# Optimization experiments

Hardware: AMD Instinct MI355X
Metric: run time of the kernel (lower is better)

Reference implementation:

```python
import jax, jax.numpy as jnp
import numpy as np

B, N, M = 8, 512, 6          # batch, num_roads, max_action
ED, SRC, OBS = 8, 64, 32     # edge_dim, source_obs_dim, obs_dim
D, H = 16, 64                # out_dim (fixed in source), MLPBase hidden


def setup_inputs() -> dict:
    key = jax.random.key(0)
    ks = jax.random.split(key, 24)
    p = lambda k, sh, s=0.05: (jax.random.normal(k, sh) * s).astype(jnp.float32)
    inp = {}
    inp['obs'] = jax.random.normal(ks[0], (B, SRC), dtype=jnp.float32)
    inp['obs_all'] = jax.random.normal(ks[1], (B, N, OBS), dtype=jnp.float32)
    inp['edge_attrs'] = jax.random.normal(ks[2], (B, N, N, ED), dtype=jnp.float32)
    inp['ridxs'] = jax.random.randint(ks[3], (B,), 0, N)
    idxs = jax.random.randint(ks[4], (N, M), 0, N)
    masks = jax.random.randint(ks[5], (N, M), 0, 2)
    inp['road_neighbor_idxs'] = idxs
    inp['road_neighbor_masks'] = masks
    # A[i, j] = 1 iff i is a (masked-valid) neighbor of j
    cols = jnp.repeat(jnp.arange(N), M)
    inp['A'] = jnp.zeros((N, N), jnp.float32).at[idxs.reshape(-1), cols].max(
        masks.reshape(-1).astype(jnp.float32))
    inp['PA'] = jnp.full((N, N), 1e-6, jnp.float32)
    # parameters (stored as (in, out); y = x @ W + b)
    inp['w_src'] = p(ks[6], (SRC, D * M)); inp['b_src'] = jnp.zeros((D * M,), jnp.float32)
    inp['w_obs'] = p(ks[7], (OBS, D));     inp['b_obs'] = jnp.zeros((D,), jnp.float32)
    inp['res_w'] = p(ks[8], (2, D, D));    inp['res_b'] = jnp.zeros((2, D), jnp.float32)
    inp['ge_we'] = p(ks[9], (2, ED, D));   inp['ge_be'] = jnp.zeros((2, D), jnp.float32)
    inp['ge_wemb'] = p(ks[10], (2, 3 * D, D)); inp['ge_bemb'] = jnp.zeros((2, D), jnp.float32)
    inp['gated_w'] = p(ks[11], (2 * D * M, 2 * D)); inp['gated_b'] = jnp.zeros((2 * D,), jnp.float32)
    inp['base_w1'] = p(ks[12], (D, H));    inp['base_b1'] = jnp.zeros((H,), jnp.float32)
    inp['base_w2'] = p(ks[13], (H, H));    inp['base_b2'] = jnp.zeros((H,), jnp.float32)
    inp['act_w'] = p(ks[14], (H, M));      inp['act_b'] = jnp.zeros((M,), jnp.float32)
    return inp


def _edge_conv_gat(x, edge_attrs, adj, we, be, wemb, bemb):
    """EdgeConvGat: emb(cat[x_i, x_j, edge_map(e)]) aggregated by adj.
    emb is linear, so split its weight and avoid the (B,N,N,3D) concat:
      sum_j adj[bij] * (x_i W1 + x_j W2 + e_ij W3 + b)
    """
    W1, W2, W3 = wemb[:D], wemb[D:2 * D], wemb[2 * D:]
    e = edge_attrs @ we + be                      # (B,N,N,D)
    ep = e @ W3                                   # (B,N,N,D)
    deg = adj.sum(-1)                             # (B,N) row-sums of adj
    return ((x @ W1) * deg[..., None]
            + jnp.einsum('bij,bjk->bik', adj, x @ W2)
            + jnp.einsum('bij,bijk->bik', adj, ep)
            + bemb * deg[..., None])


def reference(obs, obs_all, edge_attrs, ridxs, road_neighbor_idxs,
              road_neighbor_masks, A, PA, w_src, b_src, w_obs, b_obs,
              res_w, res_b, ge_we, ge_be, ge_wemb, ge_bemb,
              gated_w, gated_b, base_w1, base_b1, base_w2, base_b2,
              act_w, act_b):
    # source_obs_map / obs_map (mean_field=1 -> full obs_all)
    obs_p = obs @ w_src + b_src                   # (B, D*M)
    x = obs_all @ w_obs + b_obs                   # (B, N, D)
    # adaptive adjacency (training=False -> dropout is identity)
    adj = jnp.broadcast_to(A + PA, (obs.shape[0], N, N))
    # graph conv loop (source overwrites obs_all_adaptive each iter from the
    # same x, faithfully reproduced; only the last iteration feeds the output)
    x_adapt = x
    for i in range(2):
        res = x @ res_w[i] + res_b[i]
        agg = _edge_conv_gat(x, edge_attrs, adj, ge_we[i], ge_be[i],
                             ge_wemb[i], ge_bemb[i])
        x_adapt = jax.nn.relu(res + agg)
    # gather per-road neighbor features and mask invalid slots to -1
    idx = road_neighbor_idxs[ridxs]               # (B, M)
    mask = road_neighbor_masks[ridxs]             # (B, M)
    sel = jnp.take_along_axis(x_adapt, idx[:, :, None], axis=1)  # (B, M, D)
    sel = jnp.where(mask[..., None] == 0, -1.0, sel).reshape(obs.shape[0], -1)
    # gated fusion + MLPBase (2-layer MLP stand-in) + action head
    g = jnp.concatenate([obs_p, sel], axis=-1) @ gated_w + gated_b
    gated, gate = jnp.split(g, 2, axis=-1)
    h = gated * jax.nn.sigmoid(gate)
    h = jax.nn.relu(h @ base_w1 + base_b1)
    h = jax.nn.relu(h @ base_w2 + base_b2)        # F.relu(self.base(...))
    return h @ act_w + act_b                      # (B, M) action values
```

## Files before the change

### kernel.cpp

```cpp
#include <hip/hip_runtime.h>
#include <math.h>


constexpr int Bc   = 8;
constexpr int Nc   = 512;
constexpr int Mc   = 6;
constexpr int EDc  = 8;
constexpr int SRCc = 64;
constexpr int OBSc = 32;
constexpr int Dc   = 16;
constexpr int Hc   = 64;

__global__ __launch_bounds__(512) void anmodel_kernel(
    const float* __restrict__ obs,
    const float* __restrict__ obs_all,
    const float* __restrict__ edge_attrs,
    const int*   __restrict__ ridxs,
    const int*   __restrict__ rni,
    const int*   __restrict__ rnm,
    const float* __restrict__ A,
    const float* __restrict__ PA,
    const float* __restrict__ w_src,
    const float* __restrict__ b_src,
    const float* __restrict__ w_obs,
    const float* __restrict__ b_obs,
    const float* __restrict__ res_w,
    const float* __restrict__ res_b,
    const float* __restrict__ ge_we,
    const float* __restrict__ ge_be,
    const float* __restrict__ ge_wemb,
    const float* __restrict__ ge_bemb,
    const float* __restrict__ gated_w,
    const float* __restrict__ gated_b,
    const float* __restrict__ base_w1,
    const float* __restrict__ base_b1,
    const float* __restrict__ base_w2,
    const float* __restrict__ base_b2,
    const float* __restrict__ act_w,
    const float* __restrict__ act_b,
    float* __restrict__ out)
{
    const int b    = blockIdx.x;
    const int tid  = threadIdx.x;
    const int lane = tid & 63;
    const int wave = tid >> 6;

    __shared__ float s_x[Nc][Dc];
    __shared__ float s_w[Mc][Nc];
    __shared__ float s_wobs[OBSc][Dc];
    __shared__ float s_bobs[Dc];
    __shared__ float s_W1[Dc][Dc];
    __shared__ float s_W2[Dc][Dc];
    __shared__ float s_resw[Dc][Dc];
    __shared__ float s_resb[Dc];
    __shared__ float s_we3[EDc][Dc];
    __shared__ float s_be3[Dc];
    __shared__ float s_bemb[Dc];
    __shared__ int   s_idx[Mc];
    __shared__ int   s_msk[Mc];
    __shared__ float s_sel[Mc * Dc];
    __shared__ float s_obsp[SRCc + 32];
    __shared__ float s_h0[Dc];
    __shared__ float s_h1[Hc];
    __shared__ float s_h2[Hc];

    const float* wemb1 = ge_wemb + 3 * Dc * Dc;
    for (int t = tid; t < OBSc * Dc; t += 512) s_wobs[t / Dc][t % Dc] = w_obs[t];
    for (int t = tid; t < Dc; t += 512) {
        s_bobs[t] = b_obs[t];
        s_resb[t] = res_b[Dc + t];
        s_bemb[t] = ge_bemb[Dc + t];
        float acc = 0.f;
        #pragma unroll
        for (int k = 0; k < Dc; ++k)
            acc = fmaf(ge_be[Dc + k], wemb1[(2 * Dc + k) * Dc + t], acc);
        s_be3[t] = acc;
    }
    for (int t = tid; t < Dc * Dc; t += 512) {
        s_W1[t / Dc][t % Dc]   = wemb1[t];
        s_W2[t / Dc][t % Dc]   = wemb1[Dc * Dc + t];
        s_resw[t / Dc][t % Dc] = res_w[Dc * Dc + t];
    }
    for (int t = tid; t < EDc * Dc; t += 512) {
        const int e = t / Dc, d = t % Dc;
        float acc = 0.f;
        #pragma unroll
        for (int k = 0; k < Dc; ++k)
            acc = fmaf(ge_we[EDc * Dc + e * Dc + k], wemb1[(2 * Dc + k) * Dc + d], acc);
        s_we3[e][d] = acc;
    }
    if (tid < Mc) {
        const int r = ridxs[b];
        s_idx[tid] = rni[r * Mc + tid];
        s_msk[tid] = rnm[r * Mc + tid];
    }
    __syncthreads();

    {
        const int j = tid;
        const float* oa = obs_all + ((size_t)b * Nc + j) * OBSc;
        float o[OBSc];
        #pragma unroll
        for (int k = 0; k < OBSc; k += 4) {
            const float4 v = *reinterpret_cast<const float4*>(oa + k);
            o[k] = v.x; o[k + 1] = v.y; o[k + 2] = v.z; o[k + 3] = v.w;
        }
        float xv[Dc];
        #pragma unroll
        for (int d = 0; d < Dc; ++d) xv[d] = s_bobs[d];
        #pragma unroll
        for (int k = 0; k < OBSc; ++k) {
            const float ok = o[k];
            #pragma unroll
            for (int d = 0; d < Dc; ++d) xv[d] = fmaf(ok, s_wobs[k][d], xv[d]);
        }
        #pragma unroll
        for (int d = 0; d < Dc; ++d) s_x[j][d] = xv[d];
    }
    #pragma unroll
    for (int m = 0; m < Mc; ++m) {
        const int i = s_idx[m];
        s_w[m][tid] = A[(size_t)i * Nc + tid] + PA[(size_t)i * Nc + tid];
    }
    __syncthreads();

    if (wave < Mc) {
        const int m = wave;
        const float* __restrict__ wrow = &s_w[m][0];

        float dv = 0.f;
        #pragma unroll
        for (int t = 0; t < Nc / 64; ++t) dv += wrow[t * 64 + lane];
        #pragma unroll
        for (int s = 1; s < 64; s <<= 1) dv += __shfl_xor(dv, s);

        const int dq = lane & 15, jg = lane >> 4;
        float wx = 0.f;
        #pragma unroll 8
        for (int t = 0; t < Nc / 4; ++t) {
            const int j = t * 4 + jg;
            wx = fmaf(wrow[j], s_x[j][dq], wx);
        }
        wx += __shfl_xor(wx, 16);
        wx += __shfl_xor(wx, 32);
        float wxv[Dc];
        #pragma unroll
        for (int k = 0; k < Dc; ++k) wxv[k] = __shfl(wx, k);

        const int e8 = lane & 7, jg8 = lane >> 3;
        const int i  = s_idx[m];
        const float* __restrict__ Erow = edge_attrs + (((size_t)b * Nc + i) * Nc) * EDc;
        float ag = 0.f;
        #pragma unroll 4
        for (int t = 0; t < Nc / 8; ++t) {
            const int j = t * 8 + jg8;
            ag = fmaf(wrow[j], Erow[(size_t)j * EDc + e8], ag);
        }
        ag += __shfl_xor(ag, 8);
        ag += __shfl_xor(ag, 16);
        ag += __shfl_xor(ag, 32);
        float agv[EDc];
        #pragma unroll
        for (int e = 0; e < EDc; ++e) agv[e] = __shfl(ag, e);

        if (lane < Dc) {
            const int d = lane;
            float resv = s_resb[d];
            float w1t  = 0.f;
            float adot = 0.f;
            #pragma unroll
            for (int k = 0; k < Dc; ++k) {
                const float xik = s_x[i][k];
                resv = fmaf(xik, s_resw[k][d], resv);
                w1t  = fmaf(xik, s_W1[k][d], w1t);
                adot = fmaf(wxv[k], s_W2[k][d], adot);
            }
            float agdot = 0.f;
            #pragma unroll
            for (int e = 0; e < EDc; ++e) agdot = fmaf(agv[e], s_we3[e][d], agdot);
            float aggv = fmaf(w1t, dv, adot) + agdot + dv * (s_be3[d] + s_bemb[d]);
            float xa = resv + aggv;
            xa = xa > 0.f ? xa : 0.f;
            s_sel[m * Dc + d] = (s_msk[m] == 0) ? -1.0f : xa;
        }
    } else {
        const int t = (wave - 6) * 64 + lane;
        if (t < SRCc + 32) {
            float acc = b_src[t];
            #pragma unroll 8
            for (int s = 0; s < SRCc; ++s)
                acc = fmaf(obs[b * SRCc + s], w_src[s * 96 + t], acc);
            s_obsp[t] = acc;
        }
    }
    __syncthreads();

    if (wave == 0) {
        float gv = 0.f;
        if (lane < 32) {
            gv = gated_b[lane];
            for (int t = 0; t < 96; ++t) gv = fmaf(s_obsp[t], gated_w[t * 32 + lane], gv);
            for (int t = 0; t < 96; ++t) gv = fmaf(s_sel[t],  gated_w[(96 + t) * 32 + lane], gv);
        }
        const float gate = __shfl(gv, (lane & 15) + 16);
        if (lane < Dc) {
            s_h0[lane] = gv * (1.0f / (1.0f + expf(-gate)));
        }
    }
    __syncthreads();
    if (wave == 0) {
        float acc = base_b1[lane];
        #pragma unroll
        for (int k = 0; k < Dc; ++k) acc = fmaf(s_h0[k], base_w1[k * Hc + lane], acc);
        s_h1[lane] = acc > 0.f ? acc : 0.f;
    }
    __syncthreads();
    if (wave == 0) {
        float acc = base_b2[lane];
        #pragma unroll
        for (int k = 0; k < Hc; ++k) acc = fmaf(s_h1[k], base_w2[k * Hc + lane], acc);
        s_h2[lane] = acc > 0.f ? acc : 0.f;
    }
    __syncthreads();
    if (wave == 0 && lane < Mc) {
        float acc = act_b[lane];
        #pragma unroll
        for (int k = 0; k < Hc; ++k) acc = fmaf(s_h2[k], act_w[k * Mc + lane], acc);
        out[b * Mc + lane] = acc;
    }
}

extern "C" void kernel_launch(void* const* d_in, const int* in_sizes, int n_in,
                              void* d_out, int out_size, void* d_ws, size_t ws_size,
                              hipStream_t stream) {
    (void)in_sizes; (void)n_in; (void)d_ws; (void)ws_size; (void)out_size;
    anmodel_kernel<<<dim3(Bc), dim3(512), 0, stream>>>(
        (const float*)d_in[0],  (const float*)d_in[1],  (const float*)d_in[2],
        (const int*)  d_in[3],  (const int*)  d_in[4],  (const int*)  d_in[5],
        (const float*)d_in[6],  (const float*)d_in[7],  (const float*)d_in[8],
        (const float*)d_in[9],  (const float*)d_in[10], (const float*)d_in[11],
        (const float*)d_in[12], (const float*)d_in[13], (const float*)d_in[14],
        (const float*)d_in[15], (const float*)d_in[16], (const float*)d_in[17],
        (const float*)d_in[18], (const float*)d_in[19], (const float*)d_in[20],
        (const float*)d_in[21], (const float*)d_in[22], (const float*)d_in[23],
        (const float*)d_in[24], (const float*)d_in[25],
        (float*)d_out);
}
```

Measured before the change: 151.9 us.

## Split into per-(batch,slot) row kernel and small head kernel, reassociate obs projection

Replaces the single 8-block kernel with a 48-block kernel, one block per (batch, neighbor slot), that computes each selected row's graph-conv output. A second 8-block kernel then runs the gated fusion and MLP head. The row kernel also reorders the algebra: it aggregates raw obs_all weighted by the adjacency row and projects that sum through w_obs once, instead of projecting all 512 nodes first. This spreads the work over more CUs and cuts FMA work. The cost is a second launch and a workspace round-trip, and each block now re-reads obs_all for its batch.

```diff
diff --git a/kernel.cpp b/kernel.cpp
--- a/kernel.cpp
+++ b/kernel.cpp
@@ -11,8 +11,7 @@
 constexpr int Dc   = 16;
 constexpr int Hc   = 64;
 
-__global__ __launch_bounds__(512) void anmodel_kernel(
-    const float* __restrict__ obs,
+__global__ __launch_bounds__(256) void an_rows_kernel(
     const float* __restrict__ obs_all,
     const float* __restrict__ edge_attrs,
     const int*   __restrict__ ridxs,
@@ -20,8 +19,6 @@
     const int*   __restrict__ rnm,
     const float* __restrict__ A,
     const float* __restrict__ PA,
-    const float* __restrict__ w_src,
-    const float* __restrict__ b_src,
     const float* __restrict__ w_obs,
     const float* __restrict__ b_obs,
     const float* __restrict__ res_w,
@@ -30,6 +27,130 @@
     const float* __restrict__ ge_be,
     const float* __restrict__ ge_wemb,
     const float* __restrict__ ge_bemb,
+    float* __restrict__ sel_out)
+{
+    const int blk = blockIdx.x;
+    const int b   = blk / Mc;
+    const int m   = blk % Mc;
+    const int tid = threadIdx.x;
+
+    __shared__ float s_w[Nc];
+    __shared__ float s_woa[8][OBSc];
+    __shared__ float s_ag[32][EDc];
+    __shared__ float s_oai[OBSc];
+    __shared__ float s_woaf[OBSc];
+    __shared__ float s_agf[EDc];
+    __shared__ float s_xi[Dc];
+    __shared__ float s_wx[Dc];
+    __shared__ float s_q[Dc];
+    __shared__ float s_deg;
+    __shared__ int   s_i, s_mk;
+
+    if (tid == 0) {
+        const int r = ridxs[b];
+        s_i  = rni[r * Mc + m];
+        s_mk = rnm[r * Mc + m];
+    }
+    __syncthreads();
+    const int i = s_i;
+
+    for (int t = tid; t < Nc; t += 256)
+        s_w[t] = A[(size_t)i * Nc + t] + PA[(size_t)i * Nc + t];
+    if (tid < OBSc)
+        s_oai[tid] = obs_all[((size_t)b * Nc + i) * OBSc + tid];
+    __syncthreads();
+
+    {
+        const int d = tid & 31, jg = tid >> 5;
+        const float* __restrict__ oab = obs_all + (size_t)b * Nc * OBSc;
+        float acc = 0.f;
+        #pragma unroll 4
+        for (int t = 0; t < Nc / 8; ++t) {
+            const int j = t * 8 + jg;
+            acc = fmaf(s_w[j], oab[(size_t)j * OBSc + d], acc);
+        }
+        s_woa[jg][d] = acc;
+    }
+    {
+        const int e = tid & 7, jg = tid >> 3;
+        const float* __restrict__ Erow = edge_attrs + ((size_t)b * Nc + i) * Nc * EDc;
+        float acc = 0.f;
+        #pragma unroll 4
+        for (int t = 0; t < Nc / 32; ++t) {
+            const int j = t * 32 + jg;
+            acc = fmaf(s_w[j], Erow[(size_t)j * EDc + e], acc);
+        }
+        s_ag[jg][e] = acc;
+    }
+    if (tid < 64) {
+        float dv = 0.f;
+        #pragma unroll
+        for (int t = 0; t < Nc / 64; ++t) dv += s_w[t * 64 + tid];
+        #pragma unroll
+        for (int s = 1; s < 64; s <<= 1) dv += __shfl_xor(dv, s);
+        if (tid == 0) s_deg = dv;
+    }
+    __syncthreads();
+
+    const float deg = s_deg;
+    if (tid < OBSc) {
+        float acc = 0.f;
+        #pragma unroll
+        for (int g = 0; g < 8; ++g) acc += s_woa[g][tid];
+        s_woaf[tid] = acc;
+    } else if (tid >= 64 && tid < 64 + EDc) {
+        const int e = tid - 64;
+        float acc = 0.f;
+        #pragma unroll
+        for (int g = 0; g < 32; ++g) acc += s_ag[g][e];
+        s_agf[e] = acc;
+    } else if (tid >= 128 && tid < 128 + Dc) {
+        const int d = tid - 128;
+        float acc = b_obs[d];
+        #pragma unroll 8
+        for (int k = 0; k < OBSc; ++k) acc = fmaf(s_oai[k], w_obs[k * Dc + d], acc);
+        s_xi[d] = acc;
+    }
+    __syncthreads();
+
+    if (tid < Dc) {
+        const int d = tid;
+        float acc = deg * b_obs[d];
+        #pragma unroll 8
+        for (int k = 0; k < OBSc; ++k) acc = fmaf(s_woaf[k], w_obs[k * Dc + d], acc);
+        s_wx[d] = acc;
+    } else if (tid >= 64 && tid < 64 + Dc) {
+        const int d = tid - 64;
+        float acc = deg * ge_be[Dc + d];
+        #pragma unroll
+        for (int e = 0; e < EDc; ++e)
+            acc = fmaf(s_agf[e], ge_we[EDc * Dc + e * Dc + d], acc);
+        s_q[d] = acc;
+    }
+    __syncthreads();
+
+    if (tid < Dc) {
+        const int d = tid;
+        const float* __restrict__ wemb1 = ge_wemb + 3 * Dc * Dc;
+        float resv = res_b[Dc + d];
+        float acc  = deg * ge_bemb[Dc + d];
+        #pragma unroll
+        for (int k = 0; k < Dc; ++k) {
+            resv = fmaf(s_xi[k], res_w[Dc * Dc + k * Dc + d], resv);
+            acc  = fmaf(deg * s_xi[k], wemb1[k * Dc + d], acc);
+            acc  = fmaf(s_wx[k],       wemb1[(Dc + k) * Dc + d], acc);
+            acc  = fmaf(s_q[k],        wemb1[(2 * Dc + k) * Dc + d], acc);
+        }
+        float xa = resv + acc;
+        xa = xa > 0.f ? xa : 0.f;
+        sel_out[((size_t)b * Mc + m) * Dc + d] = (s_mk == 0) ? -1.0f : xa;
+    }
+}
+
+__global__ __launch_bounds__(128) void an_head_kernel(
+    const float* __restrict__ obs,
+    const float* __restrict__ w_src,
+    const float* __restrict__ b_src,
     const float* __restrict__ gated_w,
     const float* __restrict__ gated_b,
     const float* __restrict__ base_w1,
@@ -38,211 +159,75 @@
     const float* __restrict__ base_b2,
     const float* __restrict__ act_w,
     const float* __restrict__ act_b,
+    const float* __restrict__ sel_in,
     float* __restrict__ out)
 {
-    const int b    = blockIdx.x;
-    const int tid  = threadIdx.x;
-    const int lane = tid & 63;
-    const int wave = tid >> 6;
-
-    __shared__ float s_x[Nc][Dc];
-    __shared__ float s_w[Mc][Nc];
-    __shared__ float s_wobs[OBSc][Dc];
-    __shared__ float s_bobs[Dc];
-    __shared__ float s_W1[Dc][Dc];
-    __shared__ float s_W2[Dc][Dc];
-    __shared__ float s_resw[Dc][Dc];
-    __shared__ float s_resb[Dc];
-    __shared__ float s_we3[EDc][Dc];
-    __shared__ float s_be3[Dc];
-    __shared__ float s_bemb[Dc];
-    __shared__ int   s_idx[Mc];
-    __shared__ int   s_msk[Mc];
-    __shared__ float s_sel[Mc * Dc];
-    __shared__ float s_obsp[SRCc + 32];
-    __shared__ float s_h0[Dc];
-    __shared__ float s_h1[Hc];
-    __shared__ float s_h2[Hc];
-
-    const float* wemb1 = ge_wemb + 3 * Dc * Dc;
-    for (int t = tid; t < OBSc * Dc; t += 512) s_wobs[t / Dc][t % Dc] = w_obs[t];
-    for (int t = tid; t < Dc; t += 512) {
-        s_bobs[t] = b_obs[t];
-        s_resb[t] = res_b[Dc + t];
-        s_bemb[t] = ge_bemb[Dc + t];
-        float acc = 0.f;
-        #pragma unroll
-        for (int k = 0; k < Dc; ++k)
-            acc = fmaf(ge_be[Dc + k], wemb1[(2 * Dc + k) * Dc + t], acc);
-        s_be3[t] = acc;
-    }
-    for (int t = tid; t < Dc * Dc; t += 512) {
-        s_W1[t / Dc][t % Dc]   = wemb1[t];
-        s_W2[t / Dc][t % Dc]   = wemb1[Dc * Dc + t];
-        s_resw[t / Dc][t % Dc] = res_w[Dc * Dc + t];
-    }
-    for (int t = tid; t < EDc * Dc; t += 512) {
-        const int e = t / Dc, d = t % Dc;
-        float acc = 0.f;
-        #pragma unroll
-        for (int k = 0; k < Dc; ++k)
-            acc = fmaf(ge_we[EDc * Dc + e * Dc + k], wemb1[(2 * Dc + k) * Dc + d], acc);
-        s_we3[e][d] = acc;
-    }
+    const int b   = blockIdx.x;
+    const int tid = threadIdx.x;
+    __shared__ float s_sel[96], s_obsp[96], s_g[32], s_h0[Dc], s_h1[Hc], s_h2[Hc];
+
+    if (tid < 96) {
+        s_sel[tid] = sel_in[b * 96 + tid];
+        float acc = b_src[tid];
+        #pragma unroll 8
+        for (int s = 0; s < SRCc; ++s)
+            acc = fmaf(obs[b * SRCc + s], w_src[s * 96 + tid], acc);
+        s_obsp[tid] = acc;
+    }
+    __syncthreads();
+    if (tid < 32) {
+        float gv = gated_b[tid];
+        for (int t = 0; t < 96; ++t) gv = fmaf(s_obsp[t], gated_w[t * 32 + tid], gv);
+        for (int t = 0; t < 96; ++t) gv = fmaf(s_sel[t],  gated_w[(96 + t) * 32 + tid], gv);
+        s_g[tid] = gv;
+    }
+    __syncthreads();
+    if (tid < Dc)
+        s_h0[tid] = s_g[tid] * (1.0f / (1.0f + expf(-s_g[tid + Dc])));
+    __syncthreads();
+    if (tid < Hc) {
+        float acc = base_b1[tid];
+        #pragma unroll
+        for (int k = 0; k < Dc; ++k) acc = fmaf(s_h0[k], base_w1[k * Hc + tid], acc);
+        s_h1[tid] = acc > 0.f ? acc : 0.f;
+    }
+    __syncthreads();
+    if (tid < Hc) {
+        float acc = base_b2[tid];
+        #pragma unroll 8
+        for (int k = 0; k < Hc; ++k) acc = fmaf(s_h1[k], base_w2[k * Hc + tid], acc);
+        s_h2[tid] = acc > 0.f ? acc : 0.f;
+    }
+    __syncthreads();
     if (tid < Mc) {
-        const int r = ridxs[b];
-        s_idx[tid] = rni[r * Mc + tid];
-        s_msk[tid] = rnm[r * Mc + tid];
-    }
-    __syncthreads();
-
-    {
-        const int j = tid;
-        const float* oa = obs_all + ((size_t)b * Nc + j) * OBSc;
-        float o[OBSc];
-        #pragma unroll
-        for (int k = 0; k < OBSc; k += 4) {
-            const float4 v = *reinterpret_cast<const float4*>(oa + k);
-            o[k] = v.x; o[k + 1] = v.y; o[k + 2] = v.z; o[k + 3] = v.w;
-        }
-        float xv[Dc];
-        #pragma unroll
-        for (int d = 0; d < Dc; ++d) xv[d] = s_bobs[d];
-        #pragma unroll
-        for (int k = 0; k < OBSc; ++k) {
-            const float ok = o[k];
-            #pragma unroll
-            for (int d = 0; d < Dc; ++d) xv[d] = fmaf(ok, s_wobs[k][d], xv[d]);
-        }
-        #pragma unroll
-        for (int d = 0; d < Dc; ++d) s_x[j][d] = xv[d];
-    }
-    #pragma unroll
-    for (int m = 0; m < Mc; ++m) {
-        const int i = s_idx[m];
-        s_w[m][tid] = A[(size_t)i * Nc + tid] + PA[(size_t)i * Nc + tid];
-    }
-    __syncthreads();
-
-    if (wave < Mc) {
-        const int m = wave;
-        const float* __restrict__ wrow = &s_w[m][0];
-
-        float dv = 0.f;
-        #pragma unroll
-        for (int t = 0; t < Nc / 64; ++t) dv += wrow[t * 64 + lane];
-        #pragma unroll
-        for (int s = 1; s < 64; s <<= 1) dv += __shfl_xor(dv, s);
-
-        const int dq = lane & 15, jg = lane >> 4;
-        float wx = 0.f;
-        #pragma unroll 8
-        for (int t = 0; t < Nc / 4; ++t) {
-            const int j = t * 4 + jg;
-            wx = fmaf(wrow[j], s_x[j][dq], wx);
-        }
-        wx += __shfl_xor(wx, 16);
-        wx += __shfl_xor(wx, 32);
-        float wxv[Dc];
-        #pragma unroll
-        for (int k = 0; k < Dc; ++k) wxv[k] = __shfl(wx, k);
-
-        const int e8 = lane & 7, jg8 = lane >> 3;
-        const int i  = s_idx[m];
-        const float* __restrict__ Erow = edge_attrs + (((size_t)b * Nc + i) * Nc) * EDc;
-        float ag = 0.f;
-        #pragma unroll 4
-        for (int t = 0; t < Nc / 8; ++t) {
-            const int j = t * 8 + jg8;
-            ag = fmaf(wrow[j], Erow[(size_t)j * EDc + e8], ag);
-        }
-        ag += __shfl_xor(ag, 8);
-        ag += __shfl_xor(ag, 16);
-        ag += __shfl_xor(ag, 32);
-        float agv[EDc];
-        #pragma unroll
-        for (int e = 0; e < EDc; ++e) agv[e] = __shfl(ag, e);
-
-        if (lane < Dc) {
-            const int d = lane;
-            float resv = s_resb[d];
-            float w1t  = 0.f;
-            float adot = 0.f;
-            #pragma unroll
-            for (int k = 0; k < Dc; ++k) {
-                const float xik = s_x[i][k];
-                resv = fmaf(xik, s_resw[k][d], resv);
-                w1t  = fmaf(xik, s_W1[k][d], w1t);
-                adot = fmaf(wxv[k], s_W2[k][d], adot);
-            }
-            float agdot = 0.f;
-            #pragma unroll
-            for (int e = 0; e < EDc; ++e) agdot = fmaf(agv[e], s_we3[e][d], agdot);
-            float aggv = fmaf(w1t, dv, adot) + agdot + dv * (s_be3[d] + s_bemb[d]);
-            float xa = resv + aggv;
-            xa = xa > 0.f ? xa : 0.f;
-            s_sel[m * Dc + d] = (s_msk[m] == 0) ? -1.0f : xa;
-        }
-    } else {
-        const int t = (wave - 6) * 64 + lane;
-        if (t < SRCc + 32) {
-            float acc = b_src[t];
-            #pragma unroll 8
-            for (int s = 0; s < SRCc; ++s)
-                acc = fmaf(obs[b * SRCc + s], w_src[s * 96 + t], acc);
-            s_obsp[t] = acc;
-        }
-    }
-    __syncthreads();
-
-    if (wave == 0) {
-        float gv = 0.f;
-        if (lane < 32) {
-            gv = gated_b[lane];
-            for (int t = 0; t < 96; ++t) gv = fmaf(s_obsp[t], gated_w[t * 32 + lane], gv);
-            for (int t = 0; t < 96; ++t) gv = fmaf(s_sel[t],  gated_w[(96 + t) * 32 + lane], gv);
-        }
-        const float gate = __shfl(gv, (lane & 15) + 16);
-        if (lane < Dc) {
-            s_h0[lane] = gv * (1.0f / (1.0f + expf(-gate)));
-        }
-    }
-    __syncthreads();
-    if (wave == 0) {
-        float acc = base_b1[lane];
-        #pragma unroll
-        for (int k = 0; k < Dc; ++k) acc = fmaf(s_h0[k], base_w1[k * Hc + lane], acc);
-        s_h1[lane] = acc > 0.f ? acc : 0.f;
-    }
-    __syncthreads();
-    if (wave == 0) {
-        float acc = base_b2[lane];
-        #pragma unroll
-        for (int k = 0; k < Hc; ++k) acc = fmaf(s_h1[k], base_w2[k * Hc + lane], acc);
-        s_h2[lane] = acc > 0.f ? acc : 0.f;
-    }
-    __syncthreads();
-    if (wave == 0 && lane < Mc) {
-        float acc = act_b[lane];
-        #pragma unroll
-        for (int k = 0; k < Hc; ++k) acc = fmaf(s_h2[k], act_w[k * Mc + lane], acc);
-        out[b * Mc + lane] = acc;
+        float acc = act_b[tid];
+        #pragma unroll 8
+        for (int k = 0; k < Hc; ++k) acc = fmaf(s_h2[k], act_w[k * Mc + tid], acc);
+        out[b * Mc + tid] = acc;
     }
 }
 
 extern "C" void kernel_launch(void* const* d_in, const int* in_sizes, int n_in,
                               void* d_out, int out_size, void* d_ws, size_t ws_size,
                               hipStream_t stream) {
-    (void)in_sizes; (void)n_in; (void)d_ws; (void)ws_size; (void)out_size;
-    anmodel_kernel<<<dim3(Bc), dim3(512), 0, stream>>>(
-        (const float*)d_in[0],  (const float*)d_in[1],  (const float*)d_in[2],
-        (const int*)  d_in[3],  (const int*)  d_in[4],  (const int*)  d_in[5],
-        (const float*)d_in[6],  (const float*)d_in[7],  (const float*)d_in[8],
-        (const float*)d_in[9],  (const float*)d_in[10], (const float*)d_in[11],
-        (const float*)d_in[12], (const float*)d_in[13], (const float*)d_in[14],
-        (const float*)d_in[15], (const float*)d_in[16], (const float*)d_in[17],
-        (const float*)d_in[18], (const float*)d_in[19], (const float*)d_in[20],
-        (const float*)d_in[21], (const float*)d_in[22], (const float*)d_in[23],
+    (void)in_sizes; (void)n_in; (void)ws_size; (void)out_size;
+    float* sel_ws = (float*)d_ws;
+
+    an_rows_kernel<<<dim3(Bc * Mc), dim3(256), 0, stream>>>(
+        (const float*)d_in[1],  (const float*)d_in[2],  (const int*)d_in[3],
+        (const int*)  d_in[4],  (const int*)  d_in[5],
+        (const float*)d_in[6],  (const float*)d_in[7],
+        (const float*)d_in[10], (const float*)d_in[11],
+        (const float*)d_in[12], (const float*)d_in[13],
+        (const float*)d_in[14], (const float*)d_in[15],
+        (const float*)d_in[16], (const float*)d_in[17],
+        sel_ws);
+
+    an_head_kernel<<<dim3(Bc), dim3(128), 0, stream>>>(
+        (const float*)d_in[0],  (const float*)d_in[8],  (const float*)d_in[9],
+        (const float*)d_in[18], (const float*)d_in[19],
+        (const float*)d_in[20], (const float*)d_in[21],
+        (const float*)d_in[22], (const float*)d_in[23],
         (const float*)d_in[24], (const float*)d_in[25],
-        (float*)d_out);
+        sel_ws, (float*)d_out);
 }
```

Measured after the change: 158.6 us. 1.04x slower.
